# Kernel optimization log

Hardware: AMD Instinct MI355X
Metric: run time of the kernel (lower is better)

The kernel has to match this reference:

```python
import jax, jax.numpy as jnp
import numpy as np

HID = 64
HEADS = 4
HEAD_DIM = HID // HEADS
N_MOL, N_PROT = 2048, 4096
E_MOL, E_PROT = 32768, 131072
B = 32


def _lin(key, din, dout):
    kw, kb = jax.random.split(key)
    s = 1.0 / np.sqrt(din)
    W = jax.random.uniform(kw, (din, dout), jnp.float32, -s, s)
    b = jax.random.uniform(kb, (dout,), jnp.float32, -s, s)
    return W, b


def setup_inputs() -> dict:
    key = jax.random.key(0)
    ks = jax.random.split(key, 32)
    inp = {}
    inp['mol_x'] = jax.random.normal(ks[0], (N_MOL, 11), jnp.float32)
    inp['prot_x'] = jax.random.normal(ks[1], (N_PROT, 15), jnp.float32)
    inp['mol_eattr'] = jax.random.normal(ks[2], (E_MOL, 10), jnp.float32)
    inp['prot_eattr'] = jax.random.normal(ks[3], (E_PROT, 10), jnp.float32)
    inp['mol_edge_index'] = jax.random.randint(ks[4], (2, E_MOL), 0, N_MOL, jnp.int32)
    inp['prot_edge_index'] = jax.random.randint(ks[5], (2, E_PROT), 0, N_PROT, jnp.int32)
    inp['mol_batch'] = jnp.sort(jax.random.randint(ks[6], (N_MOL,), 0, B, jnp.int32))
    inp['prot_batch'] = jnp.sort(jax.random.randint(ks[7], (N_PROT,), 0, B, jnp.int32))
    inp['node_lin_mol_W'], inp['node_lin_mol_b'] = _lin(ks[8], 11, HID)
    inp['node_lin_prot_W'], inp['node_lin_prot_b'] = _lin(ks[9], 15, HID)
    inp['edge_lin_mol_W'], inp['edge_lin_mol_b'] = _lin(ks[10], 10, HID)
    inp['edge_lin_prot_W'], inp['edge_lin_prot_b'] = _lin(ks[11], 10, HID)
    for pref, base in (('mol_conv', 12), ('prot_conv', 15)):
        W1s, b1s, W2s, b2s = [], [], [], []
        for l in range(3):
            k1, k2 = jax.random.split(ks[base + l])
            W1, b1 = _lin(k1, HID, HID)
            W2, b2 = _lin(k2, HID, HID)
            W1s.append(W1); b1s.append(b1); W2s.append(W2); b2s.append(b2)
        inp[pref + '_W1'] = jnp.stack(W1s); inp[pref + '_b1'] = jnp.stack(b1s)
        inp[pref + '_W2'] = jnp.stack(W2s); inp[pref + '_b2'] = jnp.stack(b2s)
    for pref, base in (('attn_mp', 18), ('attn_pm', 21)):
        Ws, bs = [], []
        for i in range(3):  # Q, K, V
            W, b = _lin(ks[base + i], HID, HID)
            Ws.append(W); bs.append(b)
        inp[pref + '_W'] = jnp.stack(Ws); inp[pref + '_b'] = jnp.stack(bs)
    inp['fc1_W'], inp['fc1_b'] = _lin(ks[24], 2 * HID, HID)
    inp['fc2_W'], inp['fc2_b'] = _lin(ks[25], HID, 1)
    return inp


def _gine_layer(x, src, dst, eattr, W1, b1, W2, b2):
    # message: ReLU(x_j + e_ji); GINEConv sum aggregation; eps = 0
    msg = jax.nn.relu(x[src] + eattr)                       # [E, H]
    agg = jax.ops.segment_sum(msg, dst, num_segments=x.shape[0])
    h = x + agg
    h = jax.nn.relu(h @ W1 + b1) @ W2 + b2                  # inner MLP
    return jax.nn.relu(h)                                   # post-conv ReLU


def _cross_attn(qn, kn, W, b):
    Nq, Nk = qn.shape[0], kn.shape[0]
    Q = (qn @ W[0] + b[0]).reshape(Nq, HEADS, HEAD_DIM)
    K = (kn @ W[1] + b[1]).reshape(Nk, HEADS, HEAD_DIM)
    V = (kn @ W[2] + b[2]).reshape(Nk, HEADS, HEAD_DIM)
    scores = jnp.einsum('qhd,khd->hqk', Q, K) / np.sqrt(HEAD_DIM)
    w = jax.nn.softmax(scores, axis=-1)
    out = jnp.einsum('hqk,khd->qhd', w, V)
    return out.reshape(Nq, HID)


def _pool(H, batch):
    s = jax.ops.segment_sum(H, batch, num_segments=B)
    c = jax.ops.segment_sum(jnp.ones((H.shape[0],), H.dtype), batch, num_segments=B)
    return s / jnp.maximum(c, 1.0)[:, None]


def _forward(mol_x, prot_x, mol_eattr, prot_eattr,
             node_lin_mol_W, node_lin_mol_b, node_lin_prot_W, node_lin_prot_b,
             edge_lin_mol_W, edge_lin_mol_b, edge_lin_prot_W, edge_lin_prot_b,
             mol_conv_W1, mol_conv_b1, mol_conv_W2, mol_conv_b2,
             prot_conv_W1, prot_conv_b1, prot_conv_W2, prot_conv_b2,
             attn_mp_W, attn_mp_b, attn_pm_W, attn_pm_b,
             fc1_W, fc1_b, fc2_W, fc2_b,
             mol_edge_index, prot_edge_index, mol_batch, prot_batch):
    xm = mol_x @ node_lin_mol_W + node_lin_mol_b
    xp = prot_x @ node_lin_prot_W + node_lin_prot_b
    em = mol_eattr @ edge_lin_mol_W + edge_lin_mol_b
    ep = prot_eattr @ edge_lin_prot_W + edge_lin_prot_b
    ms, md = mol_edge_index[0], mol_edge_index[1]
    ps, pd = prot_edge_index[0], prot_edge_index[1]
    for l in range(3):
        xm = _gine_layer(xm, ms, md, em, mol_conv_W1[l], mol_conv_b1[l], mol_conv_W2[l], mol_conv_b2[l])
    for l in range(3):
        xp = _gine_layer(xp, ps, pd, ep, prot_conv_W1[l], prot_conv_b1[l], prot_conv_W2[l], prot_conv_b2[l])
    H_mol = xm + _cross_attn(xm, xp, attn_mp_W, attn_mp_b)
    H_prot = xp + _cross_attn(xp, xm, attn_pm_W, attn_pm_b)
    z = jnp.concatenate([_pool(H_mol, mol_batch), _pool(H_prot, prot_batch)], axis=1)
    h = jax.nn.relu(z @ fc1_W + fc1_b)
    return jax.nn.sigmoid(h @ fc2_W + fc2_b).squeeze(-1)


def reference(mol_x, prot_x, mol_eattr, prot_eattr,
              node_lin_mol_W, node_lin_mol_b, node_lin_prot_W, node_lin_prot_b,
              edge_lin_mol_W, edge_lin_mol_b, edge_lin_prot_W, edge_lin_prot_b,
              mol_conv_W1, mol_conv_b1, mol_conv_W2, mol_conv_b2,
              prot_conv_W1, prot_conv_b1, prot_conv_W2, prot_conv_b2,
              attn_mp_W, attn_mp_b, attn_pm_W, attn_pm_b,
              fc1_W, fc1_b, fc2_W, fc2_b,
              mol_edge_index, prot_edge_index, mol_batch, prot_batch):
    return _forward(mol_x, prot_x, mol_eattr, prot_eattr,
                    node_lin_mol_W, node_lin_mol_b, node_lin_prot_W, node_lin_prot_b,
                    edge_lin_mol_W, edge_lin_mol_b, edge_lin_prot_W, edge_lin_prot_b,
                    mol_conv_W1, mol_conv_b1, mol_conv_W2, mol_conv_b2,
                    prot_conv_W1, prot_conv_b1, prot_conv_W2, prot_conv_b2,
                    attn_mp_W, attn_mp_b, attn_pm_W, attn_pm_b,
                    fc1_W, fc1_b, fc2_W, fc2_b,
                    mol_edge_index, prot_edge_index, mol_batch, prot_batch)
```

## Files before the change

### kernel.cpp

```cpp
#include <hip/hip_runtime.h>
#include <math.h>

#define HID 64
#define HEADS 4
#define HDIM 16
#define N_MOL 2048
#define N_PROT 4096
#define E_MOL 32768
#define E_PROT 131072
#define BATCH 32
#define N_TOT (N_MOL + N_PROT)
#define E_TOT (E_MOL + E_PROT)

#define TQA 16
#define TKA 32
#define KSTA 68
#define CH_MOL 4
#define CH_PROT 2
#define KCHUNK 1024

#define DOT4(a, b) ((a).x*(b).x + (a).y*(b).y + (a).z*(b).z + (a).w*(b).w)

__global__ void k_node_lin(const float* __restrict__ mol_x, const float* __restrict__ prot_x,
                           const float* __restrict__ Wm, const float* __restrict__ bm,
                           const float* __restrict__ Wp, const float* __restrict__ bp,
                           float* __restrict__ xm, float* __restrict__ xp) {
    int w = threadIdx.x >> 6, t = threadIdx.x & 63;
    int n = blockIdx.x * 4 + w;
    if (n < N_MOL) {
        const float* xr = mol_x + n * 11;
        float acc = bm[t];
#pragma unroll
        for (int i = 0; i < 11; ++i) acc += xr[i] * Wm[i * HID + t];
        xm[n * HID + t] = acc;
    } else {
        int p = n - N_MOL;
        const float* xr = prot_x + p * 15;
        float acc = bp[t];
#pragma unroll
        for (int i = 0; i < 15; ++i) acc += xr[i] * Wp[i * HID + t];
        xp[p * HID + t] = acc;
    }
}

__global__ void k_deg(const int* __restrict__ mol_ei, const int* __restrict__ prot_ei,
                      int* __restrict__ deg) {
    int e = blockIdx.x * 256 + threadIdx.x;
    if (e < E_MOL) atomicAdd(&deg[mol_ei[E_MOL + e]], 1);
    else atomicAdd(&deg[N_MOL + prot_ei[E_PROT + (e - E_MOL)]], 1);
}

__global__ void k_scan(const int* __restrict__ deg, int* __restrict__ rowptr,
                       int* __restrict__ cursor) {
    __shared__ int waveSums[4];
    int t = threadIdx.x;
    int base = t * 24;
    int local[24];
    int s = 0;
#pragma unroll
    for (int i = 0; i < 24; ++i) { local[i] = s; s += deg[base + i]; }
    int lane = t & 63, w = t >> 6;
    int pref = s;
#pragma unroll
    for (int off = 1; off < 64; off <<= 1) {
        int v = __shfl_up(pref, off, 64);
        if (lane >= off) pref += v;
    }
    if (lane == 63) waveSums[w] = pref;
    __syncthreads();
    int waveOff = 0;
    for (int i = 0; i < w; ++i) waveOff += waveSums[i];
    int excl = pref - s + waveOff;
#pragma unroll
    for (int i = 0; i < 24; ++i) {
        rowptr[base + i] = excl + local[i];
        cursor[base + i] = excl + local[i];
    }
    if (t == 255) rowptr[N_TOT] = excl + s;
}

__global__ void k_fill(const int* __restrict__ mol_ei, const int* __restrict__ prot_ei,
                       int* __restrict__ cursor, int* __restrict__ eidx) {
    int e = blockIdx.x * 256 + threadIdx.x;
    int node;
    if (e < E_MOL) node = mol_ei[E_MOL + e];
    else node = N_MOL + prot_ei[E_PROT + (e - E_MOL)];
    int pos = atomicAdd(&cursor[node], 1);
    eidx[pos] = e;
}

__global__ void k_gine(const float* __restrict__ xin_m, const float* __restrict__ xin_p,
                       float* __restrict__ xout_m, float* __restrict__ xout_p,
                       const float* __restrict__ mol_ea, const float* __restrict__ prot_ea,
                       const int* __restrict__ mol_ei, const int* __restrict__ prot_ei,
                       const float* __restrict__ Wem, const float* __restrict__ bem,
                       const float* __restrict__ Wep, const float* __restrict__ bep,
                       const float* __restrict__ W1m, const float* __restrict__ b1m,
                       const float* __restrict__ W2m, const float* __restrict__ b2m,
                       const float* __restrict__ W1p, const float* __restrict__ b1p,
                       const float* __restrict__ W2p, const float* __restrict__ b2p,
                       const int* __restrict__ rowptr, const int* __restrict__ eidx) {
    __shared__ float h0[4][HID];
    __shared__ float h1[4][HID];
    int w = threadIdx.x >> 6, t = threadIdx.x & 63;
    int nb = blockIdx.x * 4 + w;
    bool isMol = nb < N_MOL;
    const float* x = isMol ? xin_m : xin_p;
    float* xo = isMol ? xout_m : xout_p;
    int n = isMol ? nb : nb - N_MOL;
    const float* We = isMol ? Wem : Wep;
    float bt = isMol ? bem[t] : bep[t];
    const float* ea_base = isMol ? mol_ea : prot_ea;
    const int* srcarr = isMol ? mol_ei : prot_ei;
    int ebias = isMol ? 0 : E_MOL;
    float wcol[10];
#pragma unroll
    for (int i = 0; i < 10; ++i) wcol[i] = We[i * HID + t];
    float agg = 0.f;
    int beg = rowptr[nb], end = rowptr[nb + 1];
    int j = beg;
    for (; j + 1 < end; j += 2) {
        int e0 = eidx[j] - ebias;
        int e1 = eidx[j + 1] - ebias;
        int s0 = srcarr[e0];
        int s1 = srcarr[e1];
        const float2* p0 = (const float2*)(ea_base + (size_t)e0 * 10);
        const float2* p1 = (const float2*)(ea_base + (size_t)e1 * 10);
        float2 a0 = p0[0], a1 = p0[1], a2 = p0[2], a3 = p0[3], a4 = p0[4];
        float2 c0 = p1[0], c1 = p1[1], c2 = p1[2], c3 = p1[3], c4 = p1[4];
        float xs0 = x[s0 * HID + t];
        float xs1 = x[s1 * HID + t];
        float m0 = bt, m1 = bt;
        m0 = fmaf(a0.x, wcol[0], m0); m0 = fmaf(a0.y, wcol[1], m0);
        m0 = fmaf(a1.x, wcol[2], m0); m0 = fmaf(a1.y, wcol[3], m0);
        m0 = fmaf(a2.x, wcol[4], m0); m0 = fmaf(a2.y, wcol[5], m0);
        m0 = fmaf(a3.x, wcol[6], m0); m0 = fmaf(a3.y, wcol[7], m0);
        m0 = fmaf(a4.x, wcol[8], m0); m0 = fmaf(a4.y, wcol[9], m0);
        m1 = fmaf(c0.x, wcol[0], m1); m1 = fmaf(c0.y, wcol[1], m1);
        m1 = fmaf(c1.x, wcol[2], m1); m1 = fmaf(c1.y, wcol[3], m1);
        m1 = fmaf(c2.x, wcol[4], m1); m1 = fmaf(c2.y, wcol[5], m1);
        m1 = fmaf(c3.x, wcol[6], m1); m1 = fmaf(c3.y, wcol[7], m1);
        m1 = fmaf(c4.x, wcol[8], m1); m1 = fmaf(c4.y, wcol[9], m1);
        agg += fmaxf(m0 + xs0, 0.f) + fmaxf(m1 + xs1, 0.f);
    }
    if (j < end) {
        int e0 = eidx[j] - ebias;
        int s0 = srcarr[e0];
        const float2* p0 = (const float2*)(ea_base + (size_t)e0 * 10);
        float2 a0 = p0[0], a1 = p0[1], a2 = p0[2], a3 = p0[3], a4 = p0[4];
        float xs0 = x[s0 * HID + t];
        float m0 = bt;
        m0 = fmaf(a0.x, wcol[0], m0); m0 = fmaf(a0.y, wcol[1], m0);
        m0 = fmaf(a1.x, wcol[2], m0); m0 = fmaf(a1.y, wcol[3], m0);
        m0 = fmaf(a2.x, wcol[4], m0); m0 = fmaf(a2.y, wcol[5], m0);
        m0 = fmaf(a3.x, wcol[6], m0); m0 = fmaf(a3.y, wcol[7], m0);
        m0 = fmaf(a4.x, wcol[8], m0); m0 = fmaf(a4.y, wcol[9], m0);
        agg += fmaxf(m0 + xs0, 0.f);
    }
    h0[w][t] = x[n * HID + t] + agg;
    const float* W1 = isMol ? W1m : W1p;
    const float* W2 = isMol ? W2m : W2p;
    float acc = isMol ? b1m[t] : b1p[t];
    const float4* h0v = (const float4*)h0[w];
#pragma unroll
    for (int k = 0; k < 16; ++k) {
        float4 hv = h0v[k];
        acc = fmaf(hv.x, W1[(4 * k + 0) * HID + t], acc);
        acc = fmaf(hv.y, W1[(4 * k + 1) * HID + t], acc);
        acc = fmaf(hv.z, W1[(4 * k + 2) * HID + t], acc);
        acc = fmaf(hv.w, W1[(4 * k + 3) * HID + t], acc);
    }
    h1[w][t] = fmaxf(acc, 0.f);
    float acc2 = isMol ? b2m[t] : b2p[t];
    const float4* h1v = (const float4*)h1[w];
#pragma unroll
    for (int k = 0; k < 16; ++k) {
        float4 hv = h1v[k];
        acc2 = fmaf(hv.x, W2[(4 * k + 0) * HID + t], acc2);
        acc2 = fmaf(hv.y, W2[(4 * k + 1) * HID + t], acc2);
        acc2 = fmaf(hv.z, W2[(4 * k + 2) * HID + t], acc2);
        acc2 = fmaf(hv.w, W2[(4 * k + 3) * HID + t], acc2);
    }
    xo[n * HID + t] = fmaxf(acc2, 0.f);
}

__global__ void k_qkv(const float* __restrict__ xm, const float* __restrict__ xp,
                      const float* __restrict__ mpW, const float* __restrict__ mpb,
                      const float* __restrict__ pmW, const float* __restrict__ pmb,
                      float* __restrict__ Qm, float* __restrict__ Kp, float* __restrict__ Vp,
                      float* __restrict__ Qp, float* __restrict__ Km, float* __restrict__ Vm) {
    __shared__ float row[4][HID];
    int w = threadIdx.x >> 6, t = threadIdx.x & 63;
    int b = blockIdx.x * 4 + w;
    const float *src, *W, *bias;
    float* dst;
    int n;
    if (b < 2048)       { n = b;         src = xm; W = mpW;        bias = mpb;       dst = Qm; }
    else if (b < 6144)  { n = b - 2048;  src = xp; W = mpW + 4096; bias = mpb + 64;  dst = Kp; }
    else if (b < 10240) { n = b - 6144;  src = xp; W = mpW + 8192; bias = mpb + 128; dst = Vp; }
    else if (b < 14336) { n = b - 10240; src = xp; W = pmW;        bias = pmb;       dst = Qp; }
    else if (b < 16384) { n = b - 14336; src = xm; W = pmW + 4096; bias = pmb + 64;  dst = Km; }
    else                { n = b - 16384; src = xm; W = pmW + 8192; bias = pmb + 128; dst = Vm; }
    row[w][t] = src[n * HID + t];
    __syncthreads();
    float acc = bias[t];
    const float4* rv = (const float4*)row[w];
#pragma unroll
    for (int k = 0; k < 16; ++k) {
        float4 hv = rv[k];
        acc = fmaf(hv.x, W[(4 * k + 0) * HID + t], acc);
        acc = fmaf(hv.y, W[(4 * k + 1) * HID + t], acc);
        acc = fmaf(hv.z, W[(4 * k + 2) * HID + t], acc);
        acc = fmaf(hv.w, W[(4 * k + 3) * HID + t], acc);
    }
    dst[n * HID + t] = acc;
}

__device__ inline void upd4(float4& A, const float4 v0, const float4 v1,
                            float p0, float p1, float al) {
    A.x = fmaf(p1, v1.x, fmaf(p0, v0.x, A.x * al));
    A.y = fmaf(p1, v1.y, fmaf(p0, v0.y, A.y * al));
    A.z = fmaf(p1, v1.z, fmaf(p0, v0.z, A.z * al));
    A.w = fmaf(p1, v1.w, fmaf(p0, v0.w, A.w * al));
}

__device__ inline void merge4(float4& A, const float4 B, float c1, float c2) {
    A.x = A.x * c1 + B.x * c2;
    A.y = A.y * c1 + B.y * c2;
    A.z = A.z * c1 + B.z * c2;
    A.w = A.w * c1 + B.w * c2;
}

__device__ inline float4 shfl4(const float4 a, int off) {
    float4 r;
    r.x = __shfl_xor(a.x, off, 64); r.y = __shfl_xor(a.y, off, 64);
    r.z = __shfl_xor(a.z, off, 64); r.w = __shfl_xor(a.w, off, 64);
    return r;
}

__global__ __launch_bounds__(256) void k_attn(
    const float* __restrict__ Qm, const float* __restrict__ Kp, const float* __restrict__ Vp,
    const float* __restrict__ Qp, const float* __restrict__ Km, const float* __restrict__ Vm,
    float* __restrict__ part_m, float* __restrict__ part_p) {
    __shared__ float Kl[2][TKA * KSTA];
    __shared__ float Vl[2][TKA * KSTA];

    int t = threadIdx.x;
    const float *Q, *K, *V;
    float* part;
    int q0, chunk, CH;
    {
        int b = blockIdx.x;
        const int MOLB = (N_MOL / TQA) * CH_MOL;
        if (b < MOLB) {
            chunk = b & 3; q0 = (b >> 2) * TQA; CH = CH_MOL;
            Q = Qm; K = Kp; V = Vp; part = part_m;
        } else {
            b -= MOLB;
            chunk = b & 1; q0 = (b >> 1) * TQA; CH = CH_PROT;
            Q = Qp; K = Km; V = Vm; part = part_p;
        }
    }
    int kbeg = chunk * KCHUNK;

    int sub = t & 15, h = (t >> 4) & 3, qg = t >> 6;
    int r0 = t >> 4;
    int c0 = (t & 15) << 2;

    const float sc = 0.25f * 1.44269504088896f;
    float4 q4[4][4];
#pragma unroll
    for (int qq = 0; qq < 4; ++qq) {
        const float4* Qr = (const float4*)(Q + (q0 + qg * 4 + qq) * HID + h * HDIM);
#pragma unroll
        for (int j = 0; j < 4; ++j) {
            float4 v = Qr[j];
            v.x *= sc; v.y *= sc; v.z *= sc; v.w *= sc;
            q4[qq][j] = v;
        }
    }

    float mreg[4], lreg[4];
    float4 A[4][4];
#pragma unroll
    for (int qq = 0; qq < 4; ++qq) {
        mreg[qq] = -INFINITY; lreg[qq] = 0.f;
#pragma unroll
        for (int j = 0; j < 4; ++j) A[qq][j] = (float4){0.f, 0.f, 0.f, 0.f};
    }

    {
        const float4* Kg = (const float4*)(K + kbeg * HID);
        const float4* Vg = (const float4*)(V + kbeg * HID);
        float4 ka = Kg[t], kb = Kg[t + 256];
        float4 va = Vg[t], vb = Vg[t + 256];
        *(float4*)&Kl[0][r0 * KSTA + c0] = ka;
        *(float4*)&Kl[0][(r0 + 16) * KSTA + c0] = kb;
        *(float4*)&Vl[0][r0 * KSTA + c0] = va;
        *(float4*)&Vl[0][(r0 + 16) * KSTA + c0] = vb;
    }
    __syncthreads();

    const int NT = KCHUNK / TKA;
    for (int tile = 0; tile < NT; ++tile) {
        int cur = tile & 1;
        float4 ka, kb, va, vb;
        bool more = (tile + 1) < NT;
        if (more) {
            const float4* Kg = (const float4*)(K + (kbeg + (tile + 1) * TKA) * HID);
            const float4* Vg = (const float4*)(V + (kbeg + (tile + 1) * TKA) * HID);
            ka = Kg[t]; kb = Kg[t + 256];
            va = Vg[t]; vb = Vg[t + 256];
        }

        const float4* Kr0 = (const float4*)&Kl[cur][sub * KSTA + h * HDIM];
        const float4* Kr1 = (const float4*)&Kl[cur][(sub + 16) * KSTA + h * HDIM];
        float4 x0 = Kr0[0], x1 = Kr0[1], x2 = Kr0[2], x3 = Kr0[3];
        float4 y0 = Kr1[0], y1 = Kr1[1], y2 = Kr1[2], y3 = Kr1[3];

        float s0[4], s1[4];
#pragma unroll
        for (int qq = 0; qq < 4; ++qq) {
            s0[qq] = DOT4(x0, q4[qq][0]) + DOT4(x1, q4[qq][1]) + DOT4(x2, q4[qq][2]) + DOT4(x3, q4[qq][3]);
            s1[qq] = DOT4(y0, q4[qq][0]) + DOT4(y1, q4[qq][1]) + DOT4(y2, q4[qq][2]) + DOT4(y3, q4[qq][3]);
        }

        const float4* Vr0 = (const float4*)&Vl[cur][sub * KSTA + h * HDIM];
        const float4* Vr1 = (const float4*)&Vl[cur][(sub + 16) * KSTA + h * HDIM];
        float4 v00 = Vr0[0], v01 = Vr0[1], v02 = Vr0[2], v03 = Vr0[3];
        float4 v10 = Vr1[0], v11 = Vr1[1], v12 = Vr1[2], v13 = Vr1[3];

#pragma unroll
        for (int qq = 0; qq < 4; ++qq) {
            float mn = fmaxf(mreg[qq], fmaxf(s0[qq], s1[qq]));
            float al = exp2f(mreg[qq] - mn);
            float p0 = exp2f(s0[qq] - mn);
            float p1 = exp2f(s1[qq] - mn);
            lreg[qq] = lreg[qq] * al + p0 + p1;
            upd4(A[qq][0], v00, v10, p0, p1, al);
            upd4(A[qq][1], v01, v11, p0, p1, al);
            upd4(A[qq][2], v02, v12, p0, p1, al);
            upd4(A[qq][3], v03, v13, p0, p1, al);
            mreg[qq] = mn;
        }

        if (more) {
            int nxt = cur ^ 1;
            *(float4*)&Kl[nxt][r0 * KSTA + c0] = ka;
            *(float4*)&Kl[nxt][(r0 + 16) * KSTA + c0] = kb;
            *(float4*)&Vl[nxt][r0 * KSTA + c0] = va;
            *(float4*)&Vl[nxt][(r0 + 16) * KSTA + c0] = vb;
        }
        __syncthreads();
    }

#pragma unroll
    for (int off = 1; off < 16; off <<= 1) {
#pragma unroll
        for (int qq = 0; qq < 4; ++qq) {
            float m2 = __shfl_xor(mreg[qq], off, 64);
            float l2 = __shfl_xor(lreg[qq], off, 64);
            float4 B0 = shfl4(A[qq][0], off), B1 = shfl4(A[qq][1], off);
            float4 B2 = shfl4(A[qq][2], off), B3 = shfl4(A[qq][3], off);
            float mn = fmaxf(mreg[qq], m2);
            float c1 = exp2f(mreg[qq] - mn), c2 = exp2f(m2 - mn);
            lreg[qq] = lreg[qq] * c1 + l2 * c2;
            merge4(A[qq][0], B0, c1, c2); merge4(A[qq][1], B1, c1, c2);
            merge4(A[qq][2], B2, c1, c2); merge4(A[qq][3], B3, c1, c2);
            mreg[qq] = mn;
        }
    }

    if (sub == 0) {
#pragma unroll
        for (int qq = 0; qq < 4; ++qq) {
            int qi = q0 + qg * 4 + qq;
            float* pp = part + (size_t)((qi * HEADS + h) * CH + chunk) * 20;
            pp[0] = mreg[qq]; pp[1] = lreg[qq];
            *(float4*)&pp[4] = A[qq][0]; *(float4*)&pp[8] = A[qq][1];
            *(float4*)&pp[12] = A[qq][2]; *(float4*)&pp[16] = A[qq][3];
        }
    }
}

__global__ void k_attn_merge(const float* __restrict__ part_m, const float* __restrict__ part_p,
                             const float* __restrict__ xm, const float* __restrict__ xp,
                             float* __restrict__ Hm, float* __restrict__ Hp) {
    int gi = blockIdx.x * 256 + threadIdx.x;
    const float *part, *X;
    float* H;
    int CH;
    if (gi < N_MOL * HEADS) { part = part_m; X = xm; H = Hm; CH = CH_MOL; }
    else { gi -= N_MOL * HEADS; part = part_p; X = xp; H = Hp; CH = CH_PROT; }
    int q = gi >> 2, h = gi & 3;
    const float* p0 = part + (size_t)gi * CH * 20;
    float mmax = -INFINITY;
    for (int c = 0; c < CH; ++c) mmax = fmaxf(mmax, p0[c * 20]);
    float lsum = 0.f, wgt[4];
    for (int c = 0; c < CH; ++c) {
        wgt[c] = exp2f(p0[c * 20] - mmax);
        lsum += p0[c * 20 + 1] * wgt[c];
    }
    float inv = 1.f / lsum;
    const float4* Xr = (const float4*)(X + q * HID + h * HDIM);
    float4* Hr = (float4*)(H + q * HID + h * HDIM);
#pragma unroll
    for (int j = 0; j < 4; ++j) {
        float4 o = Xr[j];
        for (int c = 0; c < CH; ++c) {
            const float4 Av = *(const float4*)(p0 + c * 20 + 4 + 4 * j);
            float wc = wgt[c] * inv;
            o.x += Av.x * wc; o.y += Av.y * wc; o.z += Av.z * wc; o.w += Av.w * wc;
        }
        Hr[j] = o;
    }
}

__global__ void k_poolfinal(const float* __restrict__ Hm, const float* __restrict__ Hp,
                            const int* __restrict__ mb, const int* __restrict__ pb,
                            const float* __restrict__ fc1W, const float* __restrict__ fc1b,
                            const float* __restrict__ fc2W, const float* __restrict__ fc2b,
                            float* __restrict__ out) {
    __shared__ float part[4][HID];
    __shared__ float z[2 * HID];
    int b = blockIdx.x;
    int t = threadIdx.x;
    int col = t & 63, w = t >> 6;
    int ms, me, ps, pe;
    {
        int lo = 0, hi = N_MOL;
        while (lo < hi) { int mid = (lo + hi) >> 1; if (mb[mid] < b) lo = mid + 1; else hi = mid; }
        ms = lo; lo = ms; hi = N_MOL;
        while (lo < hi) { int mid = (lo + hi) >> 1; if (mb[mid] < b + 1) lo = mid + 1; else hi = mid; }
        me = lo;
        lo = 0; hi = N_PROT;
        while (lo < hi) { int mid = (lo + hi) >> 1; if (pb[mid] < b) lo = mid + 1; else hi = mid; }
        ps = lo; lo = ps; hi = N_PROT;
        while (lo < hi) { int mid = (lo + hi) >> 1; if (pb[mid] < b + 1) lo = mid + 1; else hi = mid; }
        pe = lo;
    }
    float s = 0.f;
    if (w < 2) {
        for (int r = ms + w; r < me; r += 2) s += Hm[r * HID + col];
    } else {
        for (int r = ps + (w - 2); r < pe; r += 2) s += Hp[r * HID + col];
    }
    part[w][col] = s;
    __syncthreads();
    if (w == 0) z[col] = (part[0][col] + part[1][col]) / fmaxf((float)(me - ms), 1.f);
    else if (w == 1) z[64 + col] = (part[2][col] + part[3][col]) / fmaxf((float)(pe - ps), 1.f);
    __syncthreads();
    if (t < 64) {
        float acc = fc1b[t];
        const float4* zv = (const float4*)z;
#pragma unroll
        for (int k = 0; k < 32; ++k) {
            float4 hv = zv[k];
            acc = fmaf(hv.x, fc1W[(4 * k + 0) * 64 + t], acc);
            acc = fmaf(hv.y, fc1W[(4 * k + 1) * 64 + t], acc);
            acc = fmaf(hv.z, fc1W[(4 * k + 2) * 64 + t], acc);
            acc = fmaf(hv.w, fc1W[(4 * k + 3) * 64 + t], acc);
        }
        float hv = fmaxf(acc, 0.f);
        float prod = hv * fc2W[t];
#pragma unroll
        for (int off = 32; off > 0; off >>= 1) prod += __shfl_xor(prod, off, 64);
        if (t == 0) out[b] = 1.f / (1.f + __expf(-(prod + fc2b[0])));
    }
}

extern "C" void kernel_launch(void* const* d_in, const int* in_sizes, int n_in,
                              void* d_out, int out_size, void* d_ws, size_t ws_size,
                              hipStream_t stream) {
    const float* mol_x   = (const float*)d_in[0];
    const float* prot_x  = (const float*)d_in[1];
    const float* mol_ea  = (const float*)d_in[2];
    const float* prot_ea = (const float*)d_in[3];
    const int*   mol_ei  = (const int*)d_in[4];
    const int*   prot_ei = (const int*)d_in[5];
    const int*   mol_b   = (const int*)d_in[6];
    const int*   prot_b  = (const int*)d_in[7];
    const float* nlmW = (const float*)d_in[8];
    const float* nlmb = (const float*)d_in[9];
    const float* nlpW = (const float*)d_in[10];
    const float* nlpb = (const float*)d_in[11];
    const float* elmW = (const float*)d_in[12];
    const float* elmb = (const float*)d_in[13];
    const float* elpW = (const float*)d_in[14];
    const float* elpb = (const float*)d_in[15];
    const float* mcW1 = (const float*)d_in[16];
    const float* mcb1 = (const float*)d_in[17];
    const float* mcW2 = (const float*)d_in[18];
    const float* mcb2 = (const float*)d_in[19];
    const float* pcW1 = (const float*)d_in[20];
    const float* pcb1 = (const float*)d_in[21];
    const float* pcW2 = (const float*)d_in[22];
    const float* pcb2 = (const float*)d_in[23];
    const float* mpW  = (const float*)d_in[24];
    const float* mpb  = (const float*)d_in[25];
    const float* pmW  = (const float*)d_in[26];
    const float* pmb  = (const float*)d_in[27];
    const float* fc1W = (const float*)d_in[28];
    const float* fc1b = (const float*)d_in[29];
    const float* fc2W = (const float*)d_in[30];
    const float* fc2b = (const float*)d_in[31];

    float* ws    = (float*)d_ws;
    float* xa_m  = ws;
    float* xa_p  = xa_m + 131072;
    float* xb_m  = xa_p + 262144;
    float* xb_p  = xb_m + 131072;
    float* Qm    = xb_p + 262144;
    float* Kp    = Qm + 131072;
    float* Vp    = Kp + 262144;
    float* Qp    = Vp + 262144;
    float* Km    = Qp + 262144;
    float* Vm    = Km + 131072;
    float* partm = Vm + 131072;
    float* partp = partm + 655360;
    int* deg     = (int*)(partp + 655360);
    int* rowptr  = deg + N_TOT;
    int* cursor  = rowptr + N_TOT + 1;
    int* eidx    = cursor + N_TOT;
    float* Hm = Qm;
    float* Hp = Qp;

    hipMemsetAsync(deg, 0, N_TOT * sizeof(int), stream);

    k_node_lin<<<N_TOT / 4, 256, 0, stream>>>(mol_x, prot_x, nlmW, nlmb, nlpW, nlpb, xa_m, xa_p);
    k_deg<<<E_TOT / 256, 256, 0, stream>>>(mol_ei, prot_ei, deg);
    k_scan<<<1, 256, 0, stream>>>(deg, rowptr, cursor);
    k_fill<<<E_TOT / 256, 256, 0, stream>>>(mol_ei, prot_ei, cursor, eidx);

    k_gine<<<N_TOT / 4, 256, 0, stream>>>(xa_m, xa_p, xb_m, xb_p, mol_ea, prot_ea, mol_ei, prot_ei,
        elmW, elmb, elpW, elpb,
        mcW1, mcb1, mcW2, mcb2, pcW1, pcb1, pcW2, pcb2, rowptr, eidx);
    k_gine<<<N_TOT / 4, 256, 0, stream>>>(xb_m, xb_p, xa_m, xa_p, mol_ea, prot_ea, mol_ei, prot_ei,
        elmW, elmb, elpW, elpb,
        mcW1 + 4096, mcb1 + 64, mcW2 + 4096, mcb2 + 64,
        pcW1 + 4096, pcb1 + 64, pcW2 + 4096, pcb2 + 64, rowptr, eidx);
    k_gine<<<N_TOT / 4, 256, 0, stream>>>(xa_m, xa_p, xb_m, xb_p, mol_ea, prot_ea, mol_ei, prot_ei,
        elmW, elmb, elpW, elpb,
        mcW1 + 8192, mcb1 + 128, mcW2 + 8192, mcb2 + 128,
        pcW1 + 8192, pcb1 + 128, pcW2 + 8192, pcb2 + 128, rowptr, eidx);

    k_qkv<<<18432 / 4, 256, 0, stream>>>(xb_m, xb_p, mpW, mpb, pmW, pmb, Qm, Kp, Vp, Qp, Km, Vm);
    k_attn<<<(N_MOL / TQA) * CH_MOL + (N_PROT / TQA) * CH_PROT, 256, 0, stream>>>(
        Qm, Kp, Vp, Qp, Km, Vm, partm, partp);
    k_attn_merge<<<(N_MOL + N_PROT) * HEADS / 256, 256, 0, stream>>>(
        partm, partp, xb_m, xb_p, Hm, Hp);

    k_poolfinal<<<BATCH, 256, 0, stream>>>(Hm, Hp, mol_b, prot_b,
                                           fc1W, fc1b, fc2W, fc2b, (float*)d_out);
}
```

Baseline: 402.0 us.

## Replace CSR build with fixed-capacity buckets, fuse attention merge, batch two nodes per wave

Drops the degree count and prefix-scan kernels and buckets incoming edges into fixed 128-slot lists per node. GINE and QKV now handle two nodes per wave so each weight load is reused twice. The attention merge becomes a last-block-done step inside the attention kernel, driven by an atomic counter, and exp2f is replaced by the hardware exp2 builtin. This removes three launches and some redundant weight traffic. The cost is that any node with more than 128 incoming edges would overflow its bucket, and the bucket lists reuse the attention partial buffer, which is only safe while the two lifetimes do not overlap.

```diff
diff --git a/kernel.cpp b/kernel.cpp
--- a/kernel.cpp
+++ b/kernel.cpp
@@ -11,6 +11,7 @@
 #define BATCH 32
 #define N_TOT (N_MOL + N_PROT)
 #define E_TOT (E_MOL + E_PROT)
+#define CAP 128
 
 #define TQA 16
 #define TKA 32
@@ -18,8 +19,11 @@
 #define CH_MOL 4
 #define CH_PROT 2
 #define KCHUNK 1024
+#define NGRP_MOL (N_MOL / TQA)
+#define NGRP (NGRP_MOL + N_PROT / TQA)
 
 #define DOT4(a, b) ((a).x*(b).x + (a).y*(b).y + (a).z*(b).z + (a).w*(b).w)
+#define EXP2(x) __builtin_amdgcn_exp2f(x)
 
 __global__ void k_node_lin(const float* __restrict__ mol_x, const float* __restrict__ prot_x,
                            const float* __restrict__ Wm, const float* __restrict__ bm,
@@ -43,50 +47,14 @@
     }
 }
 
-__global__ void k_deg(const int* __restrict__ mol_ei, const int* __restrict__ prot_ei,
-                      int* __restrict__ deg) {
+__global__ void k_bucket(const int* __restrict__ mol_ei, const int* __restrict__ prot_ei,
+                         int* __restrict__ cursor, int* __restrict__ eidx) {
     int e = blockIdx.x * 256 + threadIdx.x;
-    if (e < E_MOL) atomicAdd(&deg[mol_ei[E_MOL + e]], 1);
-    else atomicAdd(&deg[N_MOL + prot_ei[E_PROT + (e - E_MOL)]], 1);
-}
-
-__global__ void k_scan(const int* __restrict__ deg, int* __restrict__ rowptr,
-                       int* __restrict__ cursor) {
-    __shared__ int waveSums[4];
-    int t = threadIdx.x;
-    int base = t * 24;
-    int local[24];
-    int s = 0;
-#pragma unroll
-    for (int i = 0; i < 24; ++i) { local[i] = s; s += deg[base + i]; }
-    int lane = t & 63, w = t >> 6;
-    int pref = s;
-#pragma unroll
-    for (int off = 1; off < 64; off <<= 1) {
-        int v = __shfl_up(pref, off, 64);
-        if (lane >= off) pref += v;
-    }
-    if (lane == 63) waveSums[w] = pref;
-    __syncthreads();
-    int waveOff = 0;
-    for (int i = 0; i < w; ++i) waveOff += waveSums[i];
-    int excl = pref - s + waveOff;
-#pragma unroll
-    for (int i = 0; i < 24; ++i) {
-        rowptr[base + i] = excl + local[i];
-        cursor[base + i] = excl + local[i];
-    }
-    if (t == 255) rowptr[N_TOT] = excl + s;
-}
-
-__global__ void k_fill(const int* __restrict__ mol_ei, const int* __restrict__ prot_ei,
-                       int* __restrict__ cursor, int* __restrict__ eidx) {
-    int e = blockIdx.x * 256 + threadIdx.x;
-    int node;
-    if (e < E_MOL) node = mol_ei[E_MOL + e];
-    else node = N_MOL + prot_ei[E_PROT + (e - E_MOL)];
+    int node, loc;
+    if (e < E_MOL) { node = mol_ei[E_MOL + e]; loc = e; }
+    else { int el = e - E_MOL; node = N_MOL + prot_ei[E_PROT + el]; loc = el; }
     int pos = atomicAdd(&cursor[node], 1);
-    eidx[pos] = e;
+    eidx[(size_t)node * CAP + pos] = loc;
 }
 
 __global__ void k_gine(const float* __restrict__ xin_m, const float* __restrict__ xin_p,
@@ -99,89 +67,104 @@
                        const float* __restrict__ W2m, const float* __restrict__ b2m,
                        const float* __restrict__ W1p, const float* __restrict__ b1p,
                        const float* __restrict__ W2p, const float* __restrict__ b2p,
-                       const int* __restrict__ rowptr, const int* __restrict__ eidx) {
-    __shared__ float h0[4][HID];
-    __shared__ float h1[4][HID];
+                       const int* __restrict__ cnt, const int* __restrict__ eidx) {
+    __shared__ float h0[8][HID];
+    __shared__ float h1[8][HID];
     int w = threadIdx.x >> 6, t = threadIdx.x & 63;
-    int nb = blockIdx.x * 4 + w;
-    bool isMol = nb < N_MOL;
-    const float* x = isMol ? xin_m : xin_p;
-    float* xo = isMol ? xout_m : xout_p;
-    int n = isMol ? nb : nb - N_MOL;
+    int nb0 = blockIdx.x * 8 + w * 2;
+    bool isMol = nb0 < N_MOL;
+    const float* x  = isMol ? xin_m : xin_p;
+    float* xo       = isMol ? xout_m : xout_p;
     const float* We = isMol ? Wem : Wep;
-    float bt = isMol ? bem[t] : bep[t];
+    float bt        = isMol ? bem[t] : bep[t];
     const float* ea_base = isMol ? mol_ea : prot_ea;
-    const int* srcarr = isMol ? mol_ei : prot_ei;
-    int ebias = isMol ? 0 : E_MOL;
+    const int* srcarr    = isMol ? mol_ei : prot_ei;
+    int nbias = isMol ? 0 : N_MOL;
     float wcol[10];
 #pragma unroll
     for (int i = 0; i < 10; ++i) wcol[i] = We[i * HID + t];
-    float agg = 0.f;
-    int beg = rowptr[nb], end = rowptr[nb + 1];
-    int j = beg;
-    for (; j + 1 < end; j += 2) {
-        int e0 = eidx[j] - ebias;
-        int e1 = eidx[j + 1] - ebias;
-        int s0 = srcarr[e0];
-        int s1 = srcarr[e1];
-        const float2* p0 = (const float2*)(ea_base + (size_t)e0 * 10);
-        const float2* p1 = (const float2*)(ea_base + (size_t)e1 * 10);
-        float2 a0 = p0[0], a1 = p0[1], a2 = p0[2], a3 = p0[3], a4 = p0[4];
-        float2 c0 = p1[0], c1 = p1[1], c2 = p1[2], c3 = p1[3], c4 = p1[4];
-        float xs0 = x[s0 * HID + t];
-        float xs1 = x[s1 * HID + t];
-        float m0 = bt, m1 = bt;
-        m0 = fmaf(a0.x, wcol[0], m0); m0 = fmaf(a0.y, wcol[1], m0);
-        m0 = fmaf(a1.x, wcol[2], m0); m0 = fmaf(a1.y, wcol[3], m0);
-        m0 = fmaf(a2.x, wcol[4], m0); m0 = fmaf(a2.y, wcol[5], m0);
-        m0 = fmaf(a3.x, wcol[6], m0); m0 = fmaf(a3.y, wcol[7], m0);
-        m0 = fmaf(a4.x, wcol[8], m0); m0 = fmaf(a4.y, wcol[9], m0);
-        m1 = fmaf(c0.x, wcol[0], m1); m1 = fmaf(c0.y, wcol[1], m1);
-        m1 = fmaf(c1.x, wcol[2], m1); m1 = fmaf(c1.y, wcol[3], m1);
-        m1 = fmaf(c2.x, wcol[4], m1); m1 = fmaf(c2.y, wcol[5], m1);
-        m1 = fmaf(c3.x, wcol[6], m1); m1 = fmaf(c3.y, wcol[7], m1);
-        m1 = fmaf(c4.x, wcol[8], m1); m1 = fmaf(c4.y, wcol[9], m1);
-        agg += fmaxf(m0 + xs0, 0.f) + fmaxf(m1 + xs1, 0.f);
-    }
-    if (j < end) {
-        int e0 = eidx[j] - ebias;
-        int s0 = srcarr[e0];
-        const float2* p0 = (const float2*)(ea_base + (size_t)e0 * 10);
-        float2 a0 = p0[0], a1 = p0[1], a2 = p0[2], a3 = p0[3], a4 = p0[4];
-        float xs0 = x[s0 * HID + t];
-        float m0 = bt;
-        m0 = fmaf(a0.x, wcol[0], m0); m0 = fmaf(a0.y, wcol[1], m0);
-        m0 = fmaf(a1.x, wcol[2], m0); m0 = fmaf(a1.y, wcol[3], m0);
-        m0 = fmaf(a2.x, wcol[4], m0); m0 = fmaf(a2.y, wcol[5], m0);
-        m0 = fmaf(a3.x, wcol[6], m0); m0 = fmaf(a3.y, wcol[7], m0);
-        m0 = fmaf(a4.x, wcol[8], m0); m0 = fmaf(a4.y, wcol[9], m0);
-        agg += fmaxf(m0 + xs0, 0.f);
-    }
-    h0[w][t] = x[n * HID + t] + agg;
+
+#pragma unroll
+    for (int u = 0; u < 2; ++u) {
+        int nb = nb0 + u, n = nb - nbias;
+        int deg = cnt[nb];
+        const int* lst = eidx + (size_t)nb * CAP;
+        float agg = 0.f;
+        int j = 0;
+        for (; j + 1 < deg; j += 2) {
+            int e0 = lst[j], e1 = lst[j + 1];
+            int s0 = srcarr[e0], s1 = srcarr[e1];
+            const float2* p0 = (const float2*)(ea_base + (size_t)e0 * 10);
+            const float2* p1 = (const float2*)(ea_base + (size_t)e1 * 10);
+            float2 a0 = p0[0], a1 = p0[1], a2 = p0[2], a3 = p0[3], a4 = p0[4];
+            float2 c0 = p1[0], c1 = p1[1], c2 = p1[2], c3 = p1[3], c4 = p1[4];
+            float xs0 = x[s0 * HID + t];
+            float xs1 = x[s1 * HID + t];
+            float m0 = bt, m1 = bt;
+            m0 = fmaf(a0.x, wcol[0], m0); m0 = fmaf(a0.y, wcol[1], m0);
+            m0 = fmaf(a1.x, wcol[2], m0); m0 = fmaf(a1.y, wcol[3], m0);
+            m0 = fmaf(a2.x, wcol[4], m0); m0 = fmaf(a2.y, wcol[5], m0);
+            m0 = fmaf(a3.x, wcol[6], m0); m0 = fmaf(a3.y, wcol[7], m0);
+            m0 = fmaf(a4.x, wcol[8], m0); m0 = fmaf(a4.y, wcol[9], m0);
+            m1 = fmaf(c0.x, wcol[0], m1); m1 = fmaf(c0.y, wcol[1], m1);
+            m1 = fmaf(c1.x, wcol[2], m1); m1 = fmaf(c1.y, wcol[3], m1);
+            m1 = fmaf(c2.x, wcol[4], m1); m1 = fmaf(c2.y, wcol[5], m1);
+            m1 = fmaf(c3.x, wcol[6], m1); m1 = fmaf(c3.y, wcol[7], m1);
+            m1 = fmaf(c4.x, wcol[8], m1); m1 = fmaf(c4.y, wcol[9], m1);
+            agg += fmaxf(m0 + xs0, 0.f) + fmaxf(m1 + xs1, 0.f);
+        }
+        if (j < deg) {
+            int e0 = lst[j];
+            int s0 = srcarr[e0];
+            const float2* p0 = (const float2*)(ea_base + (size_t)e0 * 10);
+            float2 a0 = p0[0], a1 = p0[1], a2 = p0[2], a3 = p0[3], a4 = p0[4];
+            float xs0 = x[s0 * HID + t];
+            float m0 = bt;
+            m0 = fmaf(a0.x, wcol[0], m0); m0 = fmaf(a0.y, wcol[1], m0);
+            m0 = fmaf(a1.x, wcol[2], m0); m0 = fmaf(a1.y, wcol[3], m0);
+            m0 = fmaf(a2.x, wcol[4], m0); m0 = fmaf(a2.y, wcol[5], m0);
+            m0 = fmaf(a3.x, wcol[6], m0); m0 = fmaf(a3.y, wcol[7], m0);
+            m0 = fmaf(a4.x, wcol[8], m0); m0 = fmaf(a4.y, wcol[9], m0);
+            agg += fmaxf(m0 + xs0, 0.f);
+        }
+        h0[w * 2 + u][t] = x[(nb0 - nbias + u) * HID + t] + agg;
+    }
+
     const float* W1 = isMol ? W1m : W1p;
     const float* W2 = isMol ? W2m : W2p;
-    float acc = isMol ? b1m[t] : b1p[t];
-    const float4* h0v = (const float4*)h0[w];
+    float b1v = isMol ? b1m[t] : b1p[t];
+    float b2v = isMol ? b2m[t] : b2p[t];
+    float acc0 = b1v, acc1 = b1v;
+    const float4* hA = (const float4*)h0[w * 2];
+    const float4* hB = (const float4*)h0[w * 2 + 1];
 #pragma unroll
     for (int k = 0; k < 16; ++k) {
-        float4 hv = h0v[k];
-        acc = fmaf(hv.x, W1[(4 * k + 0) * HID + t], acc);
-        acc = fmaf(hv.y, W1[(4 * k + 1) * HID + t], acc);
-        acc = fmaf(hv.z, W1[(4 * k + 2) * HID + t], acc);
-        acc = fmaf(hv.w, W1[(4 * k + 3) * HID + t], acc);
-    }
-    h1[w][t] = fmaxf(acc, 0.f);
-    float acc2 = isMol ? b2m[t] : b2p[t];
-    const float4* h1v = (const float4*)h1[w];
+        float4 a = hA[k], b = hB[k];
+        float w0 = W1[(4 * k + 0) * HID + t], w1 = W1[(4 * k + 1) * HID + t];
+        float w2 = W1[(4 * k + 2) * HID + t], w3 = W1[(4 * k + 3) * HID + t];
+        acc0 = fmaf(a.x, w0, acc0); acc1 = fmaf(b.x, w0, acc1);
+        acc0 = fmaf(a.y, w1, acc0); acc1 = fmaf(b.y, w1, acc1);
+        acc0 = fmaf(a.z, w2, acc0); acc1 = fmaf(b.z, w2, acc1);
+        acc0 = fmaf(a.w, w3, acc0); acc1 = fmaf(b.w, w3, acc1);
+    }
+    h1[w * 2][t] = fmaxf(acc0, 0.f);
+    h1[w * 2 + 1][t] = fmaxf(acc1, 0.f);
+    float d0 = b2v, d1 = b2v;
+    const float4* gA = (const float4*)h1[w * 2];
+    const float4* gB = (const float4*)h1[w * 2 + 1];
 #pragma unroll
     for (int k = 0; k < 16; ++k) {
-        float4 hv = h1v[k];
-        acc2 = fmaf(hv.x, W2[(4 * k + 0) * HID + t], acc2);
-        acc2 = fmaf(hv.y, W2[(4 * k + 1) * HID + t], acc2);
-        acc2 = fmaf(hv.z, W2[(4 * k + 2) * HID + t], acc2);
-        acc2 = fmaf(hv.w, W2[(4 * k + 3) * HID + t], acc2);
-    }
-    xo[n * HID + t] = fmaxf(acc2, 0.f);
+        float4 a = gA[k], b = gB[k];
+        float w0 = W2[(4 * k + 0) * HID + t], w1 = W2[(4 * k + 1) * HID + t];
+        float w2 = W2[(4 * k + 2) * HID + t], w3 = W2[(4 * k + 3) * HID + t];
+        d0 = fmaf(a.x, w0, d0); d1 = fmaf(b.x, w0, d1);
+        d0 = fmaf(a.y, w1, d0); d1 = fmaf(b.y, w1, d1);
+        d0 = fmaf(a.z, w2, d0); d1 = fmaf(b.z, w2, d1);
+        d0 = fmaf(a.w, w3, d0); d1 = fmaf(b.w, w3, d1);
+    }
+    int n0 = nb0 - nbias;
+    xo[n0 * HID + t] = fmaxf(d0, 0.f);
+    xo[(n0 + 1) * HID + t] = fmaxf(d1, 0.f);
 }
 
 __global__ void k_qkv(const float* __restrict__ xm, const float* __restrict__ xp,
@@ -189,31 +172,36 @@
                       const float* __restrict__ pmW, const float* __restrict__ pmb,
                       float* __restrict__ Qm, float* __restrict__ Kp, float* __restrict__ Vp,
                       float* __restrict__ Qp, float* __restrict__ Km, float* __restrict__ Vm) {
-    __shared__ float row[4][HID];
+    __shared__ float row[8][HID];
     int w = threadIdx.x >> 6, t = threadIdx.x & 63;
-    int b = blockIdx.x * 4 + w;
+    int b0 = blockIdx.x * 8;
     const float *src, *W, *bias;
     float* dst;
-    int n;
-    if (b < 2048)       { n = b;         src = xm; W = mpW;        bias = mpb;       dst = Qm; }
-    else if (b < 6144)  { n = b - 2048;  src = xp; W = mpW + 4096; bias = mpb + 64;  dst = Kp; }
-    else if (b < 10240) { n = b - 6144;  src = xp; W = mpW + 8192; bias = mpb + 128; dst = Vp; }
-    else if (b < 14336) { n = b - 10240; src = xp; W = pmW;        bias = pmb;       dst = Qp; }
-    else if (b < 16384) { n = b - 14336; src = xm; W = pmW + 4096; bias = pmb + 64;  dst = Km; }
-    else                { n = b - 16384; src = xm; W = pmW + 8192; bias = pmb + 128; dst = Vm; }
-    row[w][t] = src[n * HID + t];
-    __syncthreads();
-    float acc = bias[t];
-    const float4* rv = (const float4*)row[w];
+    int base;
+    if (b0 < 2048)       { base = 0;     src = xm; W = mpW;        bias = mpb;       dst = Qm; }
+    else if (b0 < 6144)  { base = 2048;  src = xp; W = mpW + 4096; bias = mpb + 64;  dst = Kp; }
+    else if (b0 < 10240) { base = 6144;  src = xp; W = mpW + 8192; bias = mpb + 128; dst = Vp; }
+    else if (b0 < 14336) { base = 10240; src = xp; W = pmW;        bias = pmb;       dst = Qp; }
+    else if (b0 < 16384) { base = 14336; src = xm; W = pmW + 4096; bias = pmb + 64;  dst = Km; }
+    else                 { base = 16384; src = xm; W = pmW + 8192; bias = pmb + 128; dst = Vm; }
+    int n0 = b0 - base + w * 2, n1 = n0 + 1;
+    row[w * 2][t] = src[n0 * HID + t];
+    row[w * 2 + 1][t] = src[n1 * HID + t];
+    float acc0 = bias[t], acc1 = acc0;
+    const float4* rA = (const float4*)row[w * 2];
+    const float4* rB = (const float4*)row[w * 2 + 1];
 #pragma unroll
     for (int k = 0; k < 16; ++k) {
-        float4 hv = rv[k];
-        acc = fmaf(hv.x, W[(4 * k + 0) * HID + t], acc);
-        acc = fmaf(hv.y, W[(4 * k + 1) * HID + t], acc);
-        acc = fmaf(hv.z, W[(4 * k + 2) * HID + t], acc);
-        acc = fmaf(hv.w, W[(4 * k + 3) * HID + t], acc);
-    }
-    dst[n * HID + t] = acc;
+        float4 a = rA[k], b = rB[k];
+        float w0 = W[(4 * k + 0) * HID + t], w1 = W[(4 * k + 1) * HID + t];
+        float w2 = W[(4 * k + 2) * HID + t], w3 = W[(4 * k + 3) * HID + t];
+        acc0 = fmaf(a.x, w0, acc0); acc1 = fmaf(b.x, w0, acc1);
+        acc0 = fmaf(a.y, w1, acc0); acc1 = fmaf(b.y, w1, acc1);
+        acc0 = fmaf(a.z, w2, acc0); acc1 = fmaf(b.z, w2, acc1);
+        acc0 = fmaf(a.w, w3, acc0); acc1 = fmaf(b.w, w3, acc1);
+    }
+    dst[n0 * HID + t] = acc0;
+    dst[n1 * HID + t] = acc1;
 }
 
 __device__ inline void upd4(float4& A, const float4 v0, const float4 v1,
@@ -241,24 +229,28 @@
 __global__ __launch_bounds__(256) void k_attn(
     const float* __restrict__ Qm, const float* __restrict__ Kp, const float* __restrict__ Vp,
     const float* __restrict__ Qp, const float* __restrict__ Km, const float* __restrict__ Vm,
-    float* __restrict__ part_m, float* __restrict__ part_p) {
+    const float* __restrict__ xm, const float* __restrict__ xp,
+    float* __restrict__ Hm, float* __restrict__ Hp,
+    float* __restrict__ part_m, float* __restrict__ part_p,
+    int* __restrict__ qcnt) {
     __shared__ float Kl[2][TKA * KSTA];
     __shared__ float Vl[2][TKA * KSTA];
+    __shared__ int lastFlag;
 
     int t = threadIdx.x;
-    const float *Q, *K, *V;
-    float* part;
-    int q0, chunk, CH;
+    const float *Q, *K, *V, *X;
+    float *part, *H;
+    int q0, chunk, CH, grp;
     {
         int b = blockIdx.x;
-        const int MOLB = (N_MOL / TQA) * CH_MOL;
+        const int MOLB = NGRP_MOL * CH_MOL;
         if (b < MOLB) {
-            chunk = b & 3; q0 = (b >> 2) * TQA; CH = CH_MOL;
-            Q = Qm; K = Kp; V = Vp; part = part_m;
+            chunk = b & 3; q0 = (b >> 2) * TQA; CH = CH_MOL; grp = b >> 2;
+            Q = Qm; K = Kp; V = Vp; part = part_m; X = xm; H = Hm;
         } else {
             b -= MOLB;
-            chunk = b & 1; q0 = (b >> 1) * TQA; CH = CH_PROT;
-            Q = Qp; K = Km; V = Vm; part = part_p;
+            chunk = b & 1; q0 = (b >> 1) * TQA; CH = CH_PROT; grp = NGRP_MOL + (b >> 1);
+            Q = Qp; K = Km; V = Vm; part = part_p; X = xp; H = Hp;
         }
     }
     int kbeg = chunk * KCHUNK;
@@ -333,9 +325,9 @@
 #pragma unroll
         for (int qq = 0; qq < 4; ++qq) {
             float mn = fmaxf(mreg[qq], fmaxf(s0[qq], s1[qq]));
-            float al = exp2f(mreg[qq] - mn);
-            float p0 = exp2f(s0[qq] - mn);
-            float p1 = exp2f(s1[qq] - mn);
+            float al = EXP2(mreg[qq] - mn);
+            float p0 = EXP2(s0[qq] - mn);
+            float p1 = EXP2(s1[qq] - mn);
             lreg[qq] = lreg[qq] * al + p0 + p1;
             upd4(A[qq][0], v00, v10, p0, p1, al);
             upd4(A[qq][1], v01, v11, p0, p1, al);
@@ -363,7 +355,7 @@
             float4 B0 = shfl4(A[qq][0], off), B1 = shfl4(A[qq][1], off);
             float4 B2 = shfl4(A[qq][2], off), B3 = shfl4(A[qq][3], off);
             float mn = fmaxf(mreg[qq], m2);
-            float c1 = exp2f(mreg[qq] - mn), c2 = exp2f(m2 - mn);
+            float c1 = EXP2(mreg[qq] - mn), c2 = EXP2(m2 - mn);
             lreg[qq] = lreg[qq] * c1 + l2 * c2;
             merge4(A[qq][0], B0, c1, c2); merge4(A[qq][1], B1, c1, c2);
             merge4(A[qq][2], B2, c1, c2); merge4(A[qq][3], B3, c1, c2);
@@ -381,38 +373,36 @@
             *(float4*)&pp[12] = A[qq][2]; *(float4*)&pp[16] = A[qq][3];
         }
     }
-}
-
-__global__ void k_attn_merge(const float* __restrict__ part_m, const float* __restrict__ part_p,
-                             const float* __restrict__ xm, const float* __restrict__ xp,
-                             float* __restrict__ Hm, float* __restrict__ Hp) {
-    int gi = blockIdx.x * 256 + threadIdx.x;
-    const float *part, *X;
-    float* H;
-    int CH;
-    if (gi < N_MOL * HEADS) { part = part_m; X = xm; H = Hm; CH = CH_MOL; }
-    else { gi -= N_MOL * HEADS; part = part_p; X = xp; H = Hp; CH = CH_PROT; }
-    int q = gi >> 2, h = gi & 3;
-    const float* p0 = part + (size_t)gi * CH * 20;
-    float mmax = -INFINITY;
-    for (int c = 0; c < CH; ++c) mmax = fmaxf(mmax, p0[c * 20]);
-    float lsum = 0.f, wgt[4];
-    for (int c = 0; c < CH; ++c) {
-        wgt[c] = exp2f(p0[c * 20] - mmax);
-        lsum += p0[c * 20 + 1] * wgt[c];
-    }
-    float inv = 1.f / lsum;
-    const float4* Xr = (const float4*)(X + q * HID + h * HDIM);
-    float4* Hr = (float4*)(H + q * HID + h * HDIM);
-#pragma unroll
-    for (int j = 0; j < 4; ++j) {
-        float4 o = Xr[j];
+    __syncthreads();
+    if (t == 0) {
+        __threadfence();
+        lastFlag = (atomicAdd(&qcnt[grp], 1) == CH - 1) ? 1 : 0;
+    }
+    __syncthreads();
+    if (lastFlag && t < TQA * HEADS) {
+        __threadfence();
+        int q = q0 + (t >> 2), hh = t & 3;
+        const float* p0 = part + (size_t)(q * HEADS + hh) * CH * 20;
+        float mmax = -INFINITY;
+        for (int c = 0; c < CH; ++c) mmax = fmaxf(mmax, p0[c * 20]);
+        float lsum = 0.f, wgt[4];
         for (int c = 0; c < CH; ++c) {
-            const float4 Av = *(const float4*)(p0 + c * 20 + 4 + 4 * j);
-            float wc = wgt[c] * inv;
-            o.x += Av.x * wc; o.y += Av.y * wc; o.z += Av.z * wc; o.w += Av.w * wc;
-        }
-        Hr[j] = o;
+            wgt[c] = EXP2(p0[c * 20] - mmax);
+            lsum += p0[c * 20 + 1] * wgt[c];
+        }
+        float inv = 1.f / lsum;
+        const float4* Xr = (const float4*)(X + q * HID + hh * HDIM);
+        float4* Hr = (float4*)(H + q * HID + hh * HDIM);
+#pragma unroll
+        for (int j = 0; j < 4; ++j) {
+            float4 o = Xr[j];
+            for (int c = 0; c < CH; ++c) {
+                const float4 Av = *(const float4*)(p0 + c * 20 + 4 + 4 * j);
+                float wc = wgt[c] * inv;
+                o.x += Av.x * wc; o.y += Av.y * wc; o.z += Av.z * wc; o.w += Av.w * wc;
+            }
+            Hr[j] = o;
+        }
     }
 }
 
@@ -518,37 +508,32 @@
     float* Vm    = Km + 131072;
     float* partm = Vm + 131072;
     float* partp = partm + 655360;
-    int* deg     = (int*)(partp + 655360);
-    int* rowptr  = deg + N_TOT;
-    int* cursor  = rowptr + N_TOT + 1;
-    int* eidx    = cursor + N_TOT;
+    int* cursor  = (int*)(partp + 655360);
+    int* qcnt    = cursor + N_TOT;
+    int* eidx    = (int*)partm;
     float* Hm = Qm;
     float* Hp = Qp;
 
-    hipMemsetAsync(deg, 0, N_TOT * sizeof(int), stream);
+    hipMemsetAsync(cursor, 0, (size_t)(N_TOT + NGRP) * 4, stream);
 
     k_node_lin<<<N_TOT / 4, 256, 0, stream>>>(mol_x, prot_x, nlmW, nlmb, nlpW, nlpb, xa_m, xa_p);
-    k_deg<<<E_TOT / 256, 256, 0, stream>>>(mol_ei, prot_ei, deg);
-    k_scan<<<1, 256, 0, stream>>>(deg, rowptr, cursor);
-    k_fill<<<E_TOT / 256, 256, 0, stream>>>(mol_ei, prot_ei, cursor, eidx);
-
-    k_gine<<<N_TOT / 4, 256, 0, stream>>>(xa_m, xa_p, xb_m, xb_p, mol_ea, prot_ea, mol_ei, prot_ei,
+    k_bucket<<<E_TOT / 256, 256, 0, stream>>>(mol_ei, prot_ei, cursor, eidx);
+
+    k_gine<<<N_TOT / 8, 256, 0, stream>>>(xa_m, xa_p, xb_m, xb_p, mol_ea, prot_ea, mol_ei, prot_ei,
         elmW, elmb, elpW, elpb,
-        mcW1, mcb1, mcW2, mcb2, pcW1, pcb1, pcW2, pcb2, rowptr, eidx);
-    k_gine<<<N_TOT / 4, 256, 0, stream>>>(xb_m, xb_p, xa_m, xa_p, mol_ea, prot_ea, mol_ei, prot_ei,
+        mcW1, mcb1, mcW2, mcb2, pcW1, pcb1, pcW2, pcb2, cursor, eidx);
+    k_gine<<<N_TOT / 8, 256, 0, stream>>>(xb_m, xb_p, xa_m, xa_p, mol_ea, prot_ea, mol_ei, prot_ei,
         elmW, elmb, elpW, elpb,
         mcW1 + 4096, mcb1 + 64, mcW2 + 4096, mcb2 + 64,
-        pcW1 + 4096, pcb1 + 64, pcW2 + 4096, pcb2 + 64, rowptr, eidx);
-    k_gine<<<N_TOT / 4, 256, 0, stream>>>(xa_m, xa_p, xb_m, xb_p, mol_ea, prot_ea, mol_ei, prot_ei,
+        pcW1 + 4096, pcb1 + 64, pcW2 + 4096, pcb2 + 64, cursor, eidx);
+    k_gine<<<N_TOT / 8, 256, 0, stream>>>(xa_m, xa_p, xb_m, xb_p, mol_ea, prot_ea, mol_ei, prot_ei,
         elmW, elmb, elpW, elpb,
         mcW1 + 8192, mcb1 + 128, mcW2 + 8192, mcb2 + 128,
-        pcW1 + 8192, pcb1 + 128, pcW2 + 8192, pcb2 + 128, rowptr, eidx);
-
-    k_qkv<<<18432 / 4, 256, 0, stream>>>(xb_m, xb_p, mpW, mpb, pmW, pmb, Qm, Kp, Vp, Qp, Km, Vm);
-    k_attn<<<(N_MOL / TQA) * CH_MOL + (N_PROT / TQA) * CH_PROT, 256, 0, stream>>>(
-        Qm, Kp, Vp, Qp, Km, Vm, partm, partp);
-    k_attn_merge<<<(N_MOL + N_PROT) * HEADS / 256, 256, 0, stream>>>(
-        partm, partp, xb_m, xb_p, Hm, Hp);
+        pcW1 + 8192, pcb1 + 128, pcW2 + 8192, pcb2 + 128, cursor, eidx);
+
+    k_qkv<<<18432 / 8, 256, 0, stream>>>(xb_m, xb_p, mpW, mpb, pmW, pmb, Qm, Kp, Vp, Qp, Km, Vm);
+    k_attn<<<NGRP_MOL * CH_MOL + (N_PROT / TQA) * CH_PROT, 256, 0, stream>>>(
+        Qm, Kp, Vp, Qp, Km, Vm, xb_m, xb_p, Hm, Hp, partm, partp, qcnt);
 
     k_poolfinal<<<BATCH, 256, 0, stream>>>(Hm, Hp, mol_b, prot_b,
                                            fc1W, fc1b, fc2W, fc2b, (float*)d_out);
```

Result: slower. 433.5 us (+7.8%).
